# Kernel optimization log

Hardware: AMD Instinct MI355X
Metric: run time of the kernel (lower is better)

The kernel has to match this reference:

```python
import jax, jax.numpy as jnp
import numpy as np

B, N_S, N_T, C, DEG = 8, 128, 128, 64, 10
NUM_STEPS, TAU, NEG = 5, 0.1, -1e30


def setup_inputs() -> dict:
    key = jax.random.key(0)
    k1, k2, k3, k4 = jax.random.split(key, 4)
    x_s = jax.random.normal(k1, (B * N_S, C), dtype=jnp.float32)
    x_t = jax.random.normal(k2, (B * N_T, C), dtype=jnp.float32)

    def make_edges(k, N):
        src = jnp.repeat(jnp.arange(B * N, dtype=jnp.int32), DEG)
        dst = (src // N) * N + jax.random.randint(k, (B * N * DEG,), 0, N, dtype=jnp.int32)
        return jnp.stack([src, dst])

    return {
        'x_s': x_s,
        'edge_index_s': make_edges(k3, N_S),
        'batch_s': jnp.arange(B * N_S, dtype=jnp.int32) // N_S,
        'x_t': x_t,
        'edge_index_t': make_edges(k4, N_T),
        'batch_t': jnp.arange(B * N_T, dtype=jnp.int32) // N_T,
    }


def _dense_adj(edge_index, N):
    # to_dense_adj with uniform batches: global node id -> (graph, local id)
    b = edge_index[0] // N
    return jnp.zeros((B, N, N), jnp.float32).at[b, edge_index[0] % N, edge_index[1] % N].set(1.0)


def _masked_sinkhorn(s, mask, num_steps, tau):
    # masked row softmax, then alternating column/row sum normalization
    out = jax.nn.softmax(jnp.where(mask, s, NEG), axis=-1)
    out = jnp.where(mask, out, 0.0) / tau
    for _ in range(num_steps):
        out = out / (out.sum(-2, keepdims=True) + 1e-8)  # c_norm @ out == column sums
        out = out / (out.sum(-1, keepdims=True) + 1e-8)  # out @ r_norm == row sums
    return out


def _forward(x_s, x_t, edge_index_s, edge_index_t):
    # include_gnn=False: h = x
    h_s = x_s.reshape(B, N_S, -1)
    h_t = x_t.reshape(B, N_T, -1)
    sim = jnp.einsum('bsc,btc->bst', h_s, h_t)  # [B,Ns,Nt]

    adj_s = _dense_adj(edge_index_s, N_S)
    adj_t = _dense_adj(edge_index_t, N_T)
    # fixed-cap neighbor lists (DEG is exact max degree by construction)
    vals_s, idx_s = jax.lax.top_k(adj_s, DEG)  # [B,Ns,DEG]
    vals_t, idx_t = jax.lax.top_k(adj_t, DEG)  # [B,Nt,DEG]
    mask_s = vals_s > 0
    mask_t = vals_t > 0

    # per-pair neighbor similarity block S_hat[b,i,j,p,q] = sim[b, ne_s(i)[p], ne_t(j)[q]]
    sim_rows = jax.vmap(lambda s, ix: s[ix])(sim, idx_s)          # [B,Ns,DEG,Nt]
    S_hat = jax.vmap(lambda r, ix: r[:, :, ix])(sim_rows, idx_t)  # [B,Ns,DEG,Nt,DEG]
    S_hat = S_hat.transpose(0, 1, 3, 2, 4)                        # [B,Ns,Nt,DEG,DEG]
    m = mask_s[:, :, None, :, None] & mask_t[:, None, :, None, :]
    S_hat = jnp.where(m, S_hat, 0.0)

    S = _masked_sinkhorn(S_hat, m, NUM_STEPS, TAU)
    opt_perm = jnp.argmax(S, axis=-1)  # [B,Ns,Nt,DEG]
    cost = jnp.take_along_axis(S_hat, opt_perm[..., None], axis=-1)[..., 0].sum(-1)  # [B,Ns,Nt]

    deg_s = mask_s.sum(-1)  # [B,Ns]
    deg_t = mask_t.sum(-1)  # [B,Nt]
    M = jnp.maximum(deg_s[:, :, None], deg_t[:, None, :]).astype(sim.dtype)
    # sim_update starts at zero and each (i,j) is written once -> update = cost/(1+M)
    sim2 = sim + cost / (1.0 + M)

    out = jax.nn.softmax(sim2, axis=-1)  # S_mask / sim_t_mask are all-True for uniform batches
    return out.reshape(B * N_S, N_T)


def reference(x_s, edge_index_s, batch_s, x_t, edge_index_t, batch_t):
    return _forward(x_s, x_t, edge_index_s, edge_index_t)
```

## Files before the change

kernel.cpp:

```cpp
#include <hip/hip_runtime.h>
#include <stdint.h>
#include <math.h>

#define NB 8
#define NN 128
#define NC 64
#define DEG 10
#define HP (DEG / 2)
#define NUM_STEPS 5

__device__ __forceinline__ float pswap(float x) {
    return __int_as_float(__builtin_amdgcn_update_dpp(
        0, __float_as_int(x), 0xB1, 0xF, 0xF, false));
}

__global__ __launch_bounds__(256, 4) void fused_kernel(
    const float* __restrict__ xs, const float* __restrict__ xt,
    const int* __restrict__ dst_s, const int* __restrict__ dst_t,
    float* __restrict__ out)
{
    __shared__ float  srow[DEG + 1][NN];
    __shared__ float  erow[DEG][NN + 1];
    __shared__ float4 xsl[DEG + 1][NC / 4];
    __shared__ float  smax[4], ssum[4];

    const int bi  = blockIdx.x;
    const int b   = bi >> 7, i = bi & 127;
    const int tid = threadIdx.x;
    const int j   = tid >> 1;
    const int h   = tid & 1;
    const int gs  = b * NN + i;
    const int gt  = b * NN + j;

    unsigned long long slo = 0ull, shi = 0ull;
    #pragma unroll
    for (int k = 0; k < DEG; ++k) {
        int d = dst_s[gs * DEG + k] & (NN - 1);
        if (d < 64) slo |= 1ull << d; else shi |= 1ull << (d - 64);
    }
    const int dsi = __popcll(slo) + __popcll(shi);

    const float4* xtr = (const float4*)(xt + (size_t)gt * NC) + h * (NC / 8);
    float4 xv[NC / 8];
    #pragma unroll
    for (int k = 0; k < NC / 8; ++k) xv[k] = xtr[k];

    if (tid < DEG) erow[tid][NN] = 0.0f;

    if (tid < (DEG + 1) * 16) {
        int r = tid >> 4, k = tid & 15;
        int node = i;
        if (r < DEG) {
            unsigned long long lo = slo, hi = shi; int sel = 0;
            #pragma unroll
            for (int q = 0; q < DEG; ++q) {
                int t;
                if (lo)      { t = __builtin_ctzll(lo);      lo &= lo - 1ull; }
                else if (hi) { t = 64 + __builtin_ctzll(hi); hi &= hi - 1ull; }
                else t = 0;
                if (q == r) sel = t;
            }
            node = sel;
        }
        if (r == DEG || r < dsi)
            xsl[r][k] = ((const float4*)(xs + (size_t)(b * NN + node) * NC))[k];
    }

    unsigned long long tlo = 0ull, thi = 0ull;
    #pragma unroll
    for (int k = 0; k < DEG; ++k) {
        int d = dst_t[gt * DEG + k] & (NN - 1);
        if (d < 64) tlo |= 1ull << d; else thi |= 1ull << (d - 64);
    }
    const int dtj = __popcll(tlo) + __popcll(thi);
    int ntq[DEG];
    {
        unsigned long long lo = tlo, hi = thi;
        #pragma unroll
        for (int q = 0; q < DEG; ++q) {
            int t;
            if (lo)      { t = __builtin_ctzll(lo);      lo &= lo - 1ull; }
            else if (hi) { t = 64 + __builtin_ctzll(hi); hi &= hi - 1ull; }
            else t = 0;
            ntq[q] = (q < dtj) ? t : NN;
        }
    }
    __syncthreads();

    #pragma unroll
    for (int r = 0; r <= DEG; ++r) {
        if (r == DEG || r < dsi) {
            float acc = 0.f;
            #pragma unroll
            for (int k = 0; k < NC / 8; ++k) {
                float4 a4 = xsl[r][h * (NC / 8) + k];
                acc += a4.x * xv[k].x + a4.y * xv[k].y + a4.z * xv[k].z + a4.w * xv[k].w;
            }
            float full = acc + pswap(acc);
            if (h == 0) {
                srow[r][j] = full;
                if (r < DEG) erow[r][j] = __expf(full);
            }
        } else {
            if (h == 0) erow[r][j] = 0.0f;
        }
    }
    __syncthreads();

    float T[HP][DEG];
    float a[HP], bvv[DEG];
    #pragma unroll
    for (int q = 0; q < DEG; ++q) bvv[q] = (q < dtj) ? 1.0f : 0.0f;

    #pragma unroll
    for (int pp = 0; pp < HP; ++pp) {
        int p = h * HP + pp;
        float sum = 0.f;
        #pragma unroll
        for (int q = 0; q < DEG; ++q) {
            float e = erow[p][ntq[q]];
            T[pp][q] = e;
            sum += e;
        }
        a[pp] = (p < dsi) ? __builtin_amdgcn_rcpf(sum) * 10.0f : 0.0f;
    }

    #pragma unroll 1
    for (int it = 0; it < NUM_STEPS; ++it) {
        float part[DEG];
        #pragma unroll
        for (int q = 0; q < DEG; ++q) {
            float cc = T[0][q] * a[0];
            #pragma unroll
            for (int pp = 1; pp < HP; ++pp) cc = fmaf(T[pp][q], a[pp], cc);
            part[q] = cc;
        }
        #pragma unroll
        for (int q = 0; q < DEG; ++q) {
            float cc = part[q] + pswap(part[q]);
            float bq = bvv[q];
            bvv[q] = (q < dtj) ? bq * __builtin_amdgcn_rcpf(fmaf(bq, cc, 1e-8f)) : 0.0f;
        }
        #pragma unroll
        for (int pp = 0; pp < HP; ++pp) {
            float r = T[pp][0] * bvv[0];
            #pragma unroll
            for (int q = 1; q < DEG; ++q) r = fmaf(T[pp][q], bvv[q], r);
            float ap = a[pp];
            int p = h * HP + pp;
            a[pp] = (p < dsi) ? ap * __builtin_amdgcn_rcpf(fmaf(ap, r, 1e-8f)) : 0.0f;
        }
    }

    float cpart = 0.f;
    #pragma unroll
    for (int pp = 0; pp < HP; ++pp) {
        int p = h * HP + pp;
        if (p < dsi) {
            float best = T[pp][0] * bvv[0];
            int   bc   = ntq[0];
            #pragma unroll
            for (int q = 1; q < DEG; ++q) {
                float vq = T[pp][q] * bvv[q];
                if (vq > best) { best = vq; bc = ntq[q]; }
            }
            cpart += srow[p][bc];
        }
    }
    float cost = cpart + pswap(cpart);

    float M = (float)((dsi > dtj) ? dsi : dtj);
    float simv = srow[DEG][j];
    float v = fmaf(cost, __builtin_amdgcn_rcpf(1.0f + M), simv);

    float wm = v;
    #pragma unroll
    for (int off = 32; off; off >>= 1) wm = fmaxf(wm, __shfl_xor(wm, off));
    int wid = tid >> 6;
    if ((tid & 63) == 0) smax[wid] = wm;
    __syncthreads();
    float bm = fmaxf(fmaxf(smax[0], smax[1]), fmaxf(smax[2], smax[3]));
    float e = __expf(v - bm);
    float wsum = e;
    #pragma unroll
    for (int off = 32; off; off >>= 1) wsum += __shfl_xor(wsum, off);
    if ((tid & 63) == 0) ssum[wid] = wsum;
    __syncthreads();
    float bs = (ssum[0] + ssum[1] + ssum[2] + ssum[3]) * 0.5f;

    if (h == 0) out[(size_t)gs * NN + j] = e * __builtin_amdgcn_rcpf(bs);
}

extern "C" void kernel_launch(void* const* d_in, const int* in_sizes, int n_in,
                              void* d_out, int out_size, void* d_ws, size_t ws_size,
                              hipStream_t stream) {
    (void)in_sizes; (void)n_in; (void)out_size; (void)d_ws; (void)ws_size;
    const float* x_s  = (const float*)d_in[0];
    const int*   ei_s = (const int*)  d_in[1];
    const float* x_t  = (const float*)d_in[3];
    const int*   ei_t = (const int*)  d_in[4];
    float* out = (float*)d_out;

    const int* dst_s = ei_s + NB * NN * DEG;
    const int* dst_t = ei_t + NB * NN * DEG;

    hipLaunchKernelGGL(fused_kernel, dim3(NB * NN), dim3(256), 0, stream,
                       x_s, x_t, dst_s, dst_t, out);
}
```

Before: 24.74 us.

## Split similarity rows across wave pairs and read source rows directly

The similarity phase is reorganized so each thread owns one target column with the full 64-channel x_t row in registers. Waves 0-1 compute neighbor rows 0-4 plus the self row, and waves 2-3 compute rows 5-9. This removes the shared-memory staging of source neighbor rows, one barrier, and the DPP half-sum. Source rows are now read directly from global memory through wave-uniform addresses. The cost is higher register pressure (16 float4s held per thread) and repeated global/cache loads of the same x_s rows across threads.

```diff
diff --git a/kernel.cpp b/kernel.cpp
--- a/kernel.cpp
+++ b/kernel.cpp
@@ -19,18 +19,14 @@
     const int* __restrict__ dst_s, const int* __restrict__ dst_t,
     float* __restrict__ out)
 {
-    __shared__ float  srow[DEG + 1][NN];
-    __shared__ float  erow[DEG][NN + 1];
-    __shared__ float4 xsl[DEG + 1][NC / 4];
-    __shared__ float  smax[4], ssum[4];
+    __shared__ float srow[DEG + 1][NN];
+    __shared__ float erow[DEG][NN + 1];
+    __shared__ float smax[4], ssum[4];
 
     const int bi  = blockIdx.x;
     const int b   = bi >> 7, i = bi & 127;
     const int tid = threadIdx.x;
-    const int j   = tid >> 1;
-    const int h   = tid & 1;
     const int gs  = b * NN + i;
-    const int gt  = b * NN + j;
 
     unsigned long long slo = 0ull, shi = 0ull;
     #pragma unroll
@@ -39,33 +35,30 @@
         if (d < 64) slo |= 1ull << d; else shi |= 1ull << (d - 64);
     }
     const int dsi = __popcll(slo) + __popcll(shi);
-
-    const float4* xtr = (const float4*)(xt + (size_t)gt * NC) + h * (NC / 8);
-    float4 xv[NC / 8];
-    #pragma unroll
-    for (int k = 0; k < NC / 8; ++k) xv[k] = xtr[k];
-
-    if (tid < DEG) erow[tid][NN] = 0.0f;
-
-    if (tid < (DEG + 1) * 16) {
-        int r = tid >> 4, k = tid & 15;
-        int node = i;
-        if (r < DEG) {
-            unsigned long long lo = slo, hi = shi; int sel = 0;
-            #pragma unroll
-            for (int q = 0; q < DEG; ++q) {
-                int t;
-                if (lo)      { t = __builtin_ctzll(lo);      lo &= lo - 1ull; }
-                else if (hi) { t = 64 + __builtin_ctzll(hi); hi &= hi - 1ull; }
-                else t = 0;
-                if (q == r) sel = t;
-            }
-            node = sel;
-        }
-        if (r == DEG || r < dsi)
-            xsl[r][k] = ((const float4*)(xs + (size_t)(b * NN + node) * NC))[k];
-    }
-
+    int sn[DEG];
+    {
+        unsigned long long lo = slo, hi = shi;
+        #pragma unroll
+        for (int q = 0; q < DEG; ++q) {
+            int t;
+            if (lo)      { t = __builtin_ctzll(lo);      lo &= lo - 1ull; }
+            else if (hi) { t = 64 + __builtin_ctzll(hi); hi &= hi - 1ull; }
+            else t = 0;
+            sn[q] = t;
+        }
+    }
+
+    const int wid = tid >> 6;
+    const int rh  = wid >> 1;
+    const int jc  = (tid & 63) | ((wid & 1) << 6);
+
+    const float4* xtr = (const float4*)(xt + (size_t)(b * NN + jc) * NC);
+    float4 xv[NC / 4];
+    #pragma unroll
+    for (int k = 0; k < NC / 4; ++k) xv[k] = xtr[k];
+
+    const int j = tid >> 1, h = tid & 1;
+    const int gt = b * NN + j;
     unsigned long long tlo = 0ull, thi = 0ull;
     #pragma unroll
     for (int k = 0; k < DEG; ++k) {
@@ -85,26 +78,45 @@
             ntq[q] = (q < dtj) ? t : NN;
         }
     }
-    __syncthreads();
-
-    #pragma unroll
-    for (int r = 0; r <= DEG; ++r) {
-        if (r == DEG || r < dsi) {
+
+    if (tid < DEG) erow[tid][NN] = 0.0f;
+
+#define SIMROW(R)                                                              \
+    {                                                                          \
+        if ((R) < dsi) {                                                       \
+            const float4* xsr =                                                \
+                (const float4*)(xs + (size_t)(b * NN + sn[(R)]) * NC);         \
+            float acc = 0.f;                                                   \
+            _Pragma("unroll")                                                  \
+            for (int k = 0; k < NC / 4; ++k) {                                 \
+                float4 a4 = xsr[k];                                            \
+                acc += a4.x * xv[k].x + a4.y * xv[k].y +                       \
+                       a4.z * xv[k].z + a4.w * xv[k].w;                        \
+            }                                                                  \
+            srow[(R)][jc] = acc;                                               \
+            erow[(R)][jc] = __expf(acc);                                       \
+        } else {                                                               \
+            erow[(R)][jc] = 0.0f;                                              \
+        }                                                                      \
+    }
+
+    if (rh == 0) {
+        SIMROW(0) SIMROW(1) SIMROW(2) SIMROW(3) SIMROW(4)
+        {
+            const float4* xsr = (const float4*)(xs + (size_t)gs * NC);
             float acc = 0.f;
             #pragma unroll
-            for (int k = 0; k < NC / 8; ++k) {
-                float4 a4 = xsl[r][h * (NC / 8) + k];
-                acc += a4.x * xv[k].x + a4.y * xv[k].y + a4.z * xv[k].z + a4.w * xv[k].w;
+            for (int k = 0; k < NC / 4; ++k) {
+                float4 a4 = xsr[k];
+                acc += a4.x * xv[k].x + a4.y * xv[k].y +
+                       a4.z * xv[k].z + a4.w * xv[k].w;
             }
-            float full = acc + pswap(acc);
-            if (h == 0) {
-                srow[r][j] = full;
-                if (r < DEG) erow[r][j] = __expf(full);
-            }
-        } else {
-            if (h == 0) erow[r][j] = 0.0f;
-        }
-    }
+            srow[DEG][jc] = acc;
+        }
+    } else {
+        SIMROW(5) SIMROW(6) SIMROW(7) SIMROW(8) SIMROW(9)
+    }
+#undef SIMROW
     __syncthreads();
 
     float T[HP][DEG];
@@ -176,15 +188,15 @@
     float wm = v;
     #pragma unroll
     for (int off = 32; off; off >>= 1) wm = fmaxf(wm, __shfl_xor(wm, off));
-    int wid = tid >> 6;
-    if ((tid & 63) == 0) smax[wid] = wm;
+    int wsl = tid >> 6;
+    if ((tid & 63) == 0) smax[wsl] = wm;
     __syncthreads();
     float bm = fmaxf(fmaxf(smax[0], smax[1]), fmaxf(smax[2], smax[3]));
     float e = __expf(v - bm);
     float wsum = e;
     #pragma unroll
     for (int off = 32; off; off >>= 1) wsum += __shfl_xor(wsum, off);
-    if ((tid & 63) == 0) ssum[wid] = wsum;
+    if ((tid & 63) == 0) ssum[wsl] = wsum;
     __syncthreads();
     float bs = (ssum[0] + ssum[1] + ssum[2] + ssum[3]) * 0.5f;
 
```

Measured after the change: 29.60 us. +19.6%, slower.
